# Kernel tuning notes

Hardware: AMD Instinct MI355X
Metric: run time of the kernel (lower is better)

The kernel has to match this reference:

```python
import jax, jax.numpy as jnp
import numpy as np

N_HEADS = 8
N_POINTS = 4


def _bilinear_sample(img, x, y):
    """img: (d, H, W); x, y: (P, H, W) float pixel coords (align_corners=True).
    Zero padding for out-of-bounds (matches F.grid_sample defaults).
    Returns (d, P, H, W)."""
    Hh, Ww = img.shape[1], img.shape[2]
    x0f = jnp.floor(x); y0f = jnp.floor(y)
    x0 = x0f.astype(jnp.int32); x1 = x0 + 1
    y0 = y0f.astype(jnp.int32); y1 = y0 + 1
    wx = x - x0f; wy = y - y0f

    def gather(yi, xi):
        valid = (yi >= 0) & (yi < Hh) & (xi >= 0) & (xi < Ww)
        yc = jnp.clip(yi, 0, Hh - 1)
        xc = jnp.clip(xi, 0, Ww - 1)
        v = img[:, yc, xc]  # (d, P, H, W)
        return v * valid[None].astype(img.dtype)

    out = (gather(y0, x0) * ((1 - wy) * (1 - wx))[None]
           + gather(y0, x1) * ((1 - wy) * wx)[None]
           + gather(y1, x0) * (wy * (1 - wx))[None]
           + gather(y1, x1) * (wy * wx)[None])
    return out


def _forward(query, key, W_off, b_off, W_proj, b_proj):
    B, C, H, W = query.shape
    nh, npts = N_HEADS, N_POINTS
    dh = C // nh
    N = H * W

    # offsets + weights from flattened query tokens
    qf = query.reshape(B, C, N).transpose(0, 2, 1)            # (B, N, C)
    ow = qf @ W_off + b_off                                    # (B, N, nh*npts*3)
    ow = ow.reshape(B, H, W, nh, npts, 3)
    offsets = ow[..., :2]                                      # (B,H,W,nh,npts,2)
    weights = jax.nn.softmax(ow[..., 2], axis=-1)              # (B,H,W,nh,npts)

    # base grid in [-1, 1], (x, y) order
    gy = jnp.linspace(-1.0, 1.0, H, dtype=query.dtype)
    gx = jnp.linspace(-1.0, 1.0, W, dtype=query.dtype)
    gyy, gxx = jnp.meshgrid(gy, gx, indexing='ij')             # (H, W)
    grid = jnp.stack([gxx, gyy], axis=-1)                      # (H, W, 2)

    locs = grid[None, :, :, None, None, :] + offsets * 0.1     # (B,H,W,nh,npts,2)
    locs = locs.transpose(0, 3, 4, 1, 2, 5)                    # (B,nh,npts,H,W,2)
    locs = locs.reshape(B * nh, npts, H, W, 2)

    # normalized -> pixel coords (align_corners=True)
    xpix = (locs[..., 0] + 1.0) * 0.5 * (W - 1)                # (B*nh, npts, H, W)
    ypix = (locs[..., 1] + 1.0) * 0.5 * (H - 1)

    key_r = key.reshape(B * nh, dh, H, W)
    sampled = jax.vmap(_bilinear_sample)(key_r, xpix, ypix)    # (B*nh, dh, npts, H, W)
    sampled = sampled.reshape(B, nh, dh, npts, H, W).transpose(0, 1, 3, 2, 4, 5)  # (B,nh,npts,dh,H,W)

    w = weights.transpose(0, 3, 4, 1, 2)[:, :, :, None, :, :]  # (B,nh,npts,1,H,W)
    out_feat = (sampled * w).sum(axis=2)                       # (B,nh,dh,H,W)
    out_feat = out_feat.reshape(B, C, N).transpose(0, 2, 1)    # (B,N,C)
    return out_feat @ W_proj + b_proj                          # (B,N,C)


def setup_inputs() -> dict:
    key0 = jax.random.key(0)
    ks = jax.random.split(key0, 6)
    B, C, H, W = 8, 256, 64, 64
    query = jax.random.normal(ks[0], (B, C, H, W), dtype=jnp.float32)
    key = jax.random.normal(ks[1], (B, C, H, W), dtype=jnp.float32)
    # small random offset net so sampling deviates from base grid (orig inits to 0)
    W_off = jax.random.normal(ks[2], (C, N_HEADS * N_POINTS * 3), dtype=jnp.float32) * 0.01
    b_off = jax.random.normal(ks[3], (N_HEADS * N_POINTS * 3,), dtype=jnp.float32) * 0.01
    W_proj = jax.random.normal(ks[4], (C, C), dtype=jnp.float32) * (1.0 / np.sqrt(C))
    b_proj = jnp.zeros((C,), dtype=jnp.float32)
    return {"query": query, "key": key, "W_off": W_off, "b_off": b_off,
            "W_proj": W_proj, "b_proj": b_proj}


def reference(query, key, W_off, b_off, W_proj, b_proj):
    return _forward(query, key, W_off, b_off, W_proj, b_proj)
```

## Files before the change

### kernel.cpp

```cpp
#include <hip/hip_runtime.h>

#define NH   8
#define NPTS 4
#define BB   8
#define CCH  256
#define HH   64
#define WW   64
#define NPIX 4096
#define DH   32

__global__ __launch_bounds__(256)
void kA_gemm(const float* __restrict__ query, const float* __restrict__ W_off,
             const float* __restrict__ b_off, float4* __restrict__ coords)
{
    __shared__ float a_lds[64][68];
    __shared__ float w_lds[64][100];

    const int t    = threadIdx.x;
    const int bid  = blockIdx.x;
    const int sbid = (bid & 7) * 64 + (bid >> 3);
    const int m0   = sbid * 64;
    const int b    = m0 >> 12;
    const int n0   = m0 & (NPIX - 1);
    const float* qbase = query + (size_t)b * CCH * NPIX + n0;

    const int kg = t >> 7;
    const int tl = t & 127;
    const int tm = tl >> 3;
    const int tj = tl & 7;

    float acc[4][12];
#pragma unroll
    for (int i = 0; i < 4; ++i)
#pragma unroll
        for (int j = 0; j < 12; ++j) acc[i][j] = 0.f;

    for (int kc = 0; kc < 128; kc += 32) {
        float4 a[4];
#pragma unroll
        for (int ii = 0; ii < 4; ++ii) {
            const int idx = t + ii * 256;
            const int lr = idx >> 4, m4 = idx & 15;
            const int gk = ((lr >> 5) << 7) + kc + (lr & 31);
            a[ii] = *(const float4*)(qbase + (size_t)gk * NPIX + (m4 << 2));
        }
        float4 w[6];
#pragma unroll
        for (int ii = 0; ii < 6; ++ii) {
            const int idx = t + ii * 256;
            const int lr = idx / 24, q = idx - lr * 24;
            const int gk = ((lr >> 5) << 7) + kc + (lr & 31);
            w[ii] = *(const float4*)(W_off + (size_t)gk * 96 + (q << 2));
        }
        __syncthreads();
#pragma unroll
        for (int ii = 0; ii < 4; ++ii) {
            const int idx = t + ii * 256;
            *(float4*)&a_lds[idx >> 4][(idx & 15) << 2] = a[ii];
        }
#pragma unroll
        for (int ii = 0; ii < 6; ++ii) {
            const int idx = t + ii * 256;
            const int lr = idx / 24, q = idx - lr * 24;
            *(float4*)&w_lds[lr][q << 2] = w[ii];
        }
        __syncthreads();

        const int kr0 = kg << 5;
#pragma unroll
        for (int kk = 0; kk < 32; ++kk) {
            const int kr = kr0 + kk;
            const float4 av = *(const float4*)&a_lds[kr][tm << 2];
            const float4 w0 = *(const float4*)&w_lds[kr][tj * 12];
            const float4 w1 = *(const float4*)&w_lds[kr][tj * 12 + 4];
            const float4 w2 = *(const float4*)&w_lds[kr][tj * 12 + 8];
            const float ar[4]  = {av.x, av.y, av.z, av.w};
            const float wr[12] = {w0.x, w0.y, w0.z, w0.w,
                                  w1.x, w1.y, w1.z, w1.w,
                                  w2.x, w2.y, w2.z, w2.w};
#pragma unroll
            for (int i = 0; i < 4; ++i)
#pragma unroll
                for (int j = 0; j < 12; ++j)
                    acc[i][j] = fmaf(ar[i], wr[j], acc[i][j]);
        }
    }

    __syncthreads();
    if (kg == 0) {
#pragma unroll
        for (int i = 0; i < 4; ++i)
#pragma unroll
            for (int jq = 0; jq < 3; ++jq) {
                float4 v = make_float4(acc[i][jq * 4 + 0], acc[i][jq * 4 + 1],
                                       acc[i][jq * 4 + 2], acc[i][jq * 4 + 3]);
                *(float4*)&w_lds[(tm << 2) + i][tj * 12 + (jq << 2)] = v;
            }
    }
    __syncthreads();
    if (kg == 1) {
#pragma unroll
        for (int i = 0; i < 4; ++i)
#pragma unroll
            for (int jq = 0; jq < 3; ++jq) {
                const float4 v = *(const float4*)&w_lds[(tm << 2) + i][tj * 12 + (jq << 2)];
                acc[i][jq * 4 + 0] += v.x;
                acc[i][jq * 4 + 1] += v.y;
                acc[i][jq * 4 + 2] += v.z;
                acc[i][jq * 4 + 3] += v.w;
            }

        float bo[12];
#pragma unroll
        for (int j = 0; j < 12; ++j) bo[j] = b_off[tj * 12 + j];

#pragma unroll
        for (int i = 0; i < 4; ++i) {
            const int g = m0 + (tm << 2) + i;
            const int n = g & (NPIX - 1);
            const float fx = (float)(n & 63), fy = (float)(n >> 6);

            float ox[4], oy[4], l[4];
#pragma unroll
            for (int p = 0; p < 4; ++p) {
                ox[p] = acc[i][p * 3 + 0] + bo[p * 3 + 0];
                oy[p] = acc[i][p * 3 + 1] + bo[p * 3 + 1];
                l[p]  = acc[i][p * 3 + 2] + bo[p * 3 + 2];
            }
            float m = fmaxf(fmaxf(l[0], l[1]), fmaxf(l[2], l[3]));
            float e[4], s = 0.f;
#pragma unroll
            for (int p = 0; p < 4; ++p) { e[p] = __expf(l[p] - m); s += e[p]; }
            const float inv = 1.f / s;

            float4* cp = coords + ((size_t)g * NH + tj) * NPTS;
#pragma unroll
            for (int p = 0; p < 4; ++p)
                cp[p] = make_float4(fx + ox[p] * 3.15f, fy + oy[p] * 3.15f,
                                    e[p] * inv, 0.f);
        }
    }
}

__global__ __launch_bounds__(256)
void kT_transpose(const float* __restrict__ key, float* __restrict__ keyT)
{
    __shared__ float tile[64][65];
    int bid = blockIdx.x;
    const int nt = bid & 63; bid >>= 6;
    const int ct = bid & 3;  bid >>= 2;
    const int b  = bid;
    const int n0 = nt * 64, c0 = ct * 64;
    const int t = threadIdx.x;

    const float* src = key + ((size_t)b * CCH + c0) * NPIX + n0;
#pragma unroll
    for (int ii = 0; ii < 4; ++ii) {
        int idx = t + ii * 256;
        int cc = idx >> 4, q = idx & 15;
        float4 v = *(const float4*)(src + (size_t)cc * NPIX + (q << 2));
        tile[cc][(q << 2) + 0] = v.x;
        tile[cc][(q << 2) + 1] = v.y;
        tile[cc][(q << 2) + 2] = v.z;
        tile[cc][(q << 2) + 3] = v.w;
    }
    __syncthreads();
    float* dst = keyT + ((size_t)(b * NPIX + n0)) * CCH + c0;
#pragma unroll
    for (int ii = 0; ii < 4; ++ii) {
        int idx = t + ii * 256;
        int nn = idx >> 4, q = idx & 15;
        float4 v = make_float4(tile[(q << 2) + 0][nn], tile[(q << 2) + 1][nn],
                               tile[(q << 2) + 2][nn], tile[(q << 2) + 3][nn]);
        *(float4*)(dst + (size_t)nn * CCH + (q << 2)) = v;
    }
}

__global__ __launch_bounds__(256)
void kB_gather(const float* __restrict__ keyT, const float4* __restrict__ coords,
               float* __restrict__ feat)
{
    const int bid  = blockIdx.x;
    const int sbid = (bid & 7) * 1024 + (bid >> 3);

    const int t  = threadIdx.x;
    const int wv = t >> 6, l = t & 63;
    const int g  = sbid * 4 + wv;
    const int b  = g >> 12;
    const int head = l >> 3;
    const int cl   = (l & 7) << 2;
    const int c    = head * DH + cl;

    const float*  kb = keyT + (((size_t)b << 12)) * CCH;
    const float4* cp = coords + ((size_t)g * NH + head) * NPTS;

    float4 acc = make_float4(0.f, 0.f, 0.f, 0.f);
#pragma unroll
    for (int pt = 0; pt < 4; ++pt) {
        float4 co = cp[pt];
        float xp = co.x, yp = co.y, wgt = co.z;
        float x0f = floorf(xp), y0f = floorf(yp);
        int   x0  = (int)x0f,  y0  = (int)y0f;
        float wx  = xp - x0f,  wy  = yp - y0f;
#pragma unroll
        for (int cr = 0; cr < 4; ++cr) {
            int   xi = x0 + (cr & 1);
            int   yi = y0 + (cr >> 1);
            float wc = ((cr & 1) ? wx : 1.f - wx) * ((cr >> 1) ? wy : 1.f - wy);
            bool  valid = (xi >= 0) && (xi < WW) && (yi >= 0) && (yi < HH);
            int   xc = min(max(xi, 0), WW - 1);
            int   yc = min(max(yi, 0), HH - 1);
            float ww = valid ? (wgt * wc) : 0.f;
            float4 v = *(const float4*)(kb + ((size_t)((yc << 6) + xc)) * CCH + c);
            acc.x = fmaf(ww, v.x, acc.x);
            acc.y = fmaf(ww, v.y, acc.y);
            acc.z = fmaf(ww, v.z, acc.z);
            acc.w = fmaf(ww, v.w, acc.w);
        }
    }
    *(float4*)(feat + (size_t)g * CCH + c) = acc;
}

__global__ __launch_bounds__(256)
void kB_sample(const float* __restrict__ key, const float4* __restrict__ coords,
               float* __restrict__ feat)
{
    __shared__ float cx[4][64], cy[4][64], cw[4][64];

    const int t = threadIdx.x;
    int bi = blockIdx.x;
    const int y    = bi & 63; bi >>= 6;
    const int head = bi & 7;  bi >>= 3;
    const int b    = bi;

    {
        const int xx = t >> 2, pt = t & 3;
        float4 v = coords[((size_t)(b * NPIX + y * WW + xx) * NH + head) * NPTS + pt];
        cx[pt][xx] = v.x; cy[pt][xx] = v.y; cw[pt][xx] = v.z;
    }
    __syncthreads();

    const int x  = t & 63;
    const int cg = t >> 6;
    const int c0 = head * DH + cg * 8;
    const float* kbase = key + ((size_t)b * CCH + c0) * NPIX;

    float acc[8];
#pragma unroll
    for (int i = 0; i < 8; ++i) acc[i] = 0.f;

#pragma unroll
    for (int pt = 0; pt < 4; ++pt) {
        float xp = cx[pt][x], yp = cy[pt][x], wgt = cw[pt][x];
        float x0f = floorf(xp), y0f = floorf(yp);
        int   x0  = (int)x0f,  y0  = (int)y0f;
        float wx  = xp - x0f,  wy  = yp - y0f;
#pragma unroll
        for (int cr = 0; cr < 4; ++cr) {
            int   xi = x0 + (cr & 1);
            int   yi = y0 + (cr >> 1);
            float wc = ((cr & 1) ? wx : 1.f - wx) * ((cr >> 1) ? wy : 1.f - wy);
            bool  valid = (xi >= 0) && (xi < WW) && (yi >= 0) && (yi < HH);
            int   xc = min(max(xi, 0), WW - 1);
            int   yc = min(max(yi, 0), HH - 1);
            const float* p = kbase + yc * WW + xc;
            float ww = valid ? (wgt * wc) : 0.f;
#pragma unroll
            for (int c = 0; c < 8; ++c)
                acc[c] = fmaf(ww, p[(size_t)c * NPIX], acc[c]);
        }
    }

    float* fp = feat + (size_t)(b * NPIX + y * WW + x) * CCH + c0;
    *(float4*)fp       = make_float4(acc[0], acc[1], acc[2], acc[3]);
    *(float4*)(fp + 4) = make_float4(acc[4], acc[5], acc[6], acc[7]);
}

__global__ __launch_bounds__(256)
void kC_proj(const float* __restrict__ feat, const float* __restrict__ W_proj,
             const float* __restrict__ b_proj, float* __restrict__ out)
{
    __shared__ float a_lds[64][36];
    __shared__ float b_lds[32][128];

    const int t    = threadIdx.x;
    const int bid  = blockIdx.x;
    const int sbid = (bid & 7) * 128 + (bid >> 3);
    const int mb = sbid >> 1;
    const int nb = sbid & 1;
    const int m0 = mb * 64, n0 = nb * 128;

    const int tm = t >> 4, tn = t & 15;

    float acc[4][8];
#pragma unroll
    for (int i = 0; i < 4; ++i)
#pragma unroll
        for (int j = 0; j < 8; ++j) acc[i][j] = 0.f;

    for (int kc = 0; kc < 256; kc += 32) {
        float4 a[2];
#pragma unroll
        for (int ii = 0; ii < 2; ++ii) {
            const int idx = t + ii * 256;
            a[ii] = *(const float4*)(feat + (size_t)(m0 + (idx >> 3)) * 256
                                     + kc + ((idx & 7) << 2));
        }
        float4 w[4];
#pragma unroll
        for (int ii = 0; ii < 4; ++ii) {
            const int idx = t + ii * 256;
            w[ii] = *(const float4*)(W_proj + (size_t)(kc + (idx >> 5)) * 256
                                     + n0 + ((idx & 31) << 2));
        }
        __syncthreads();
#pragma unroll
        for (int ii = 0; ii < 2; ++ii) {
            const int idx = t + ii * 256;
            *(float4*)&a_lds[idx >> 3][(idx & 7) << 2] = a[ii];
        }
#pragma unroll
        for (int ii = 0; ii < 4; ++ii) {
            const int idx = t + ii * 256;
            *(float4*)&b_lds[idx >> 5][(idx & 31) << 2] = w[ii];
        }
        __syncthreads();
#pragma unroll
        for (int k4 = 0; k4 < 8; ++k4) {
            float ar[4][4];
#pragma unroll
            for (int i = 0; i < 4; ++i) {
                const float4 av = *(const float4*)&a_lds[(tm << 2) + i][k4 << 2];
                ar[i][0] = av.x; ar[i][1] = av.y; ar[i][2] = av.z; ar[i][3] = av.w;
            }
#pragma unroll
            for (int kk = 0; kk < 4; ++kk) {
                const int k = (k4 << 2) + kk;
                const float4 bv0 = *(const float4*)&b_lds[k][tn << 2];
                const float4 bv1 = *(const float4*)&b_lds[k][64 + (tn << 2)];
                const float br[8] = {bv0.x, bv0.y, bv0.z, bv0.w,
                                     bv1.x, bv1.y, bv1.z, bv1.w};
#pragma unroll
                for (int i = 0; i < 4; ++i)
#pragma unroll
                    for (int j = 0; j < 8; ++j)
                        acc[i][j] = fmaf(ar[i][kk], br[j], acc[i][j]);
            }
        }
    }

    const float4 bp0 = *(const float4*)(b_proj + n0 + (tn << 2));
    const float4 bp1 = *(const float4*)(b_proj + n0 + 64 + (tn << 2));
#pragma unroll
    for (int i = 0; i < 4; ++i) {
        float* op = out + (size_t)(m0 + (tm << 2) + i) * 256 + n0;
        *(float4*)(op + (tn << 2)) =
            make_float4(acc[i][0] + bp0.x, acc[i][1] + bp0.y,
                        acc[i][2] + bp0.z, acc[i][3] + bp0.w);
        *(float4*)(op + 64 + (tn << 2)) =
            make_float4(acc[i][4] + bp1.x, acc[i][5] + bp1.y,
                        acc[i][6] + bp1.z, acc[i][7] + bp1.w);
    }
}

extern "C" void kernel_launch(void* const* d_in, const int* in_sizes, int n_in,
                              void* d_out, int out_size, void* d_ws, size_t ws_size,
                              hipStream_t stream)
{
    const float* query  = (const float*)d_in[0];
    const float* key    = (const float*)d_in[1];
    const float* W_off  = (const float*)d_in[2];
    const float* b_off  = (const float*)d_in[3];
    const float* W_proj = (const float*)d_in[4];
    const float* b_proj = (const float*)d_in[5];
    float* out = (float*)d_out;

    const size_t keyT_bytes   = (size_t)BB * NPIX * CCH * sizeof(float);
    const size_t coords_bytes = (size_t)BB * NPIX * NH * NPTS * sizeof(float4);
    const size_t feat_bytes   = (size_t)BB * NPIX * CCH * sizeof(float);

    if (ws_size >= keyT_bytes + coords_bytes + feat_bytes) {
        float*  keyT   = (float*)d_ws;
        float4* coords = (float4*)((char*)d_ws + keyT_bytes);
        float*  feat   = (float*)((char*)d_ws + keyT_bytes + coords_bytes);

        kA_gemm<<<(BB * NPIX) / 64, 256, 0, stream>>>(query, W_off, b_off, coords);
        kT_transpose<<<BB * 4 * 64, 256, 0, stream>>>(key, keyT);
        kB_gather<<<(BB * NPIX) / 4, 256, 0, stream>>>(keyT, coords, feat);
        kC_proj<<<(BB * NPIX / 64) * 2, 256, 0, stream>>>(feat, W_proj, b_proj, out);
    } else {
        float4* coords = (float4*)d_ws;
        float*  feat   = (float*)((char*)d_ws + coords_bytes);

        kA_gemm<<<(BB * NPIX) / 64, 256, 0, stream>>>(query, W_off, b_off, coords);
        kB_sample<<<BB * NH * HH, 256, 0, stream>>>(key, coords, feat);
        kC_proj<<<(BB * NPIX / 64) * 2, 256, 0, stream>>>(feat, W_proj, b_proj, out);
    }
}
```

Before: 269.9 us.

## Use split-bf16 MFMA for output projection and drop fallback sampler path

Replaces the FP32 SIMT output-projection GEMM with a bf16 MFMA kernel that keeps roughly FP32 accuracy by splitting each operand into high and low bf16 parts and summing three products. The gather kernel now writes the features as bf16 high/low halves, and a small new kernel transposes and splits W_proj, reusing the keyT workspace once the gather has finished. This aims to move the projection's arithmetic onto the matrix cores and cut bytes read from feat, at the cost of three MFMAs per tile and an extra launch. The smaller-workspace fallback path is removed, so the code now assumes the workspace is large enough.

```diff
diff --git a/kernel.cpp b/kernel.cpp
--- a/kernel.cpp
+++ b/kernel.cpp
@@ -1,4 +1,5 @@
 #include <hip/hip_runtime.h>
+#include <hip/hip_bf16.h>
 
 #define NH   8
 #define NPTS 4
@@ -8,6 +9,16 @@
 #define WW   64
 #define NPIX 4096
 #define DH   32
+
+typedef __attribute__((ext_vector_type(8))) short bf16x8;
+typedef __attribute__((ext_vector_type(4))) float f32x4;
+
+__device__ __forceinline__ ushort f2bf(float x) {
+    union { __hip_bfloat16 b; ushort u; } c; c.b = __float2bfloat16(x); return c.u;
+}
+__device__ __forceinline__ float bf2f(ushort u) {
+    union { __hip_bfloat16 b; ushort u; } c; c.u = u; return __bfloat162float(c.b);
+}
 
 __global__ __launch_bounds__(256)
 void kA_gemm(const float* __restrict__ query, const float* __restrict__ W_off,
@@ -120,17 +131,17 @@
             const int n = g & (NPIX - 1);
             const float fx = (float)(n & 63), fy = (float)(n >> 6);
 
-            float ox[4], oy[4], l[4];
+            float ox[4], oy[4], lg[4];
 #pragma unroll
             for (int p = 0; p < 4; ++p) {
                 ox[p] = acc[i][p * 3 + 0] + bo[p * 3 + 0];
                 oy[p] = acc[i][p * 3 + 1] + bo[p * 3 + 1];
-                l[p]  = acc[i][p * 3 + 2] + bo[p * 3 + 2];
+                lg[p] = acc[i][p * 3 + 2] + bo[p * 3 + 2];
             }
-            float m = fmaxf(fmaxf(l[0], l[1]), fmaxf(l[2], l[3]));
+            float m = fmaxf(fmaxf(lg[0], lg[1]), fmaxf(lg[2], lg[3]));
             float e[4], s = 0.f;
 #pragma unroll
-            for (int p = 0; p < 4; ++p) { e[p] = __expf(l[p] - m); s += e[p]; }
+            for (int p = 0; p < 4; ++p) { e[p] = __expf(lg[p] - m); s += e[p]; }
             const float inv = 1.f / s;
 
             float4* cp = coords + ((size_t)g * NH + tj) * NPTS;
@@ -178,7 +189,7 @@
 
 __global__ __launch_bounds__(256)
 void kB_gather(const float* __restrict__ keyT, const float4* __restrict__ coords,
-               float* __restrict__ feat)
+               ushort* __restrict__ featH, ushort* __restrict__ featL)
 {
     const int bid  = blockIdx.x;
     const int sbid = (bid & 7) * 1024 + (bid >> 3);
@@ -218,148 +229,141 @@
             acc.w = fmaf(ww, v.w, acc.w);
         }
     }
-    *(float4*)(feat + (size_t)g * CCH + c) = acc;
+    const float a4[4] = {acc.x, acc.y, acc.z, acc.w};
+    ushort hs[4], ls[4];
+#pragma unroll
+    for (int j = 0; j < 4; ++j) {
+        hs[j] = f2bf(a4[j]);
+        ls[j] = f2bf(a4[j] - bf2f(hs[j]));
+    }
+    *(ushort4*)(featH + (size_t)g * CCH + c) = make_ushort4(hs[0], hs[1], hs[2], hs[3]);
+    *(ushort4*)(featL + (size_t)g * CCH + c) = make_ushort4(ls[0], ls[1], ls[2], ls[3]);
 }
 
 __global__ __launch_bounds__(256)
-void kB_sample(const float* __restrict__ key, const float4* __restrict__ coords,
-               float* __restrict__ feat)
-{
-    __shared__ float cx[4][64], cy[4][64], cw[4][64];
-
-    const int t = threadIdx.x;
-    int bi = blockIdx.x;
-    const int y    = bi & 63; bi >>= 6;
-    const int head = bi & 7;  bi >>= 3;
-    const int b    = bi;
-
-    {
-        const int xx = t >> 2, pt = t & 3;
-        float4 v = coords[((size_t)(b * NPIX + y * WW + xx) * NH + head) * NPTS + pt];
-        cx[pt][xx] = v.x; cy[pt][xx] = v.y; cw[pt][xx] = v.z;
+void kW_conv(const float* __restrict__ W, ushort* __restrict__ WTh,
+             ushort* __restrict__ WTl)
+{
+    __shared__ float tile[64][65];
+    const int t  = threadIdx.x;
+    const int kt = blockIdx.x >> 2, nt = blockIdx.x & 3;
+    const int k0 = kt * 64, n0 = nt * 64;
+
+    const float* src = W + (size_t)k0 * 256 + n0;
+#pragma unroll
+    for (int ii = 0; ii < 4; ++ii) {
+        int idx = t + ii * 256;
+        int kk = idx >> 4, q = idx & 15;
+        float4 v = *(const float4*)(src + (size_t)kk * 256 + (q << 2));
+        tile[kk][(q << 2) + 0] = v.x;
+        tile[kk][(q << 2) + 1] = v.y;
+        tile[kk][(q << 2) + 2] = v.z;
+        tile[kk][(q << 2) + 3] = v.w;
     }
     __syncthreads();
-
-    const int x  = t & 63;
-    const int cg = t >> 6;
-    const int c0 = head * DH + cg * 8;
-    const float* kbase = key + ((size_t)b * CCH + c0) * NPIX;
-
-    float acc[8];
-#pragma unroll
-    for (int i = 0; i < 8; ++i) acc[i] = 0.f;
-
-#pragma unroll
-    for (int pt = 0; pt < 4; ++pt) {
-        float xp = cx[pt][x], yp = cy[pt][x], wgt = cw[pt][x];
-        float x0f = floorf(xp), y0f = floorf(yp);
-        int   x0  = (int)x0f,  y0  = (int)y0f;
-        float wx  = xp - x0f,  wy  = yp - y0f;
-#pragma unroll
-        for (int cr = 0; cr < 4; ++cr) {
-            int   xi = x0 + (cr & 1);
-            int   yi = y0 + (cr >> 1);
-            float wc = ((cr & 1) ? wx : 1.f - wx) * ((cr >> 1) ? wy : 1.f - wy);
-            bool  valid = (xi >= 0) && (xi < WW) && (yi >= 0) && (yi < HH);
-            int   xc = min(max(xi, 0), WW - 1);
-            int   yc = min(max(yi, 0), HH - 1);
-            const float* p = kbase + yc * WW + xc;
-            float ww = valid ? (wgt * wc) : 0.f;
-#pragma unroll
-            for (int c = 0; c < 8; ++c)
-                acc[c] = fmaf(ww, p[(size_t)c * NPIX], acc[c]);
-        }
-    }
-
-    float* fp = feat + (size_t)(b * NPIX + y * WW + x) * CCH + c0;
-    *(float4*)fp       = make_float4(acc[0], acc[1], acc[2], acc[3]);
-    *(float4*)(fp + 4) = make_float4(acc[4], acc[5], acc[6], acc[7]);
+#pragma unroll
+    for (int ii = 0; ii < 4; ++ii) {
+        int idx = t + ii * 256;
+        int nn = idx >> 4, q = idx & 15;
+        float xs[4] = { tile[(q << 2) + 0][nn], tile[(q << 2) + 1][nn],
+                        tile[(q << 2) + 2][nn], tile[(q << 2) + 3][nn] };
+        ushort hs[4], ls[4];
+#pragma unroll
+        for (int j = 0; j < 4; ++j) {
+            hs[j] = f2bf(xs[j]);
+            ls[j] = f2bf(xs[j] - bf2f(hs[j]));
+        }
+        *(ushort4*)(WTh + (size_t)(n0 + nn) * 256 + k0 + (q << 2)) =
+            make_ushort4(hs[0], hs[1], hs[2], hs[3]);
+        *(ushort4*)(WTl + (size_t)(n0 + nn) * 256 + k0 + (q << 2)) =
+            make_ushort4(ls[0], ls[1], ls[2], ls[3]);
+    }
 }
 
 __global__ __launch_bounds__(256)
-void kC_proj(const float* __restrict__ feat, const float* __restrict__ W_proj,
+void kC_mfma(const ushort* __restrict__ featH, const ushort* __restrict__ featL,
+             const ushort* __restrict__ WTh, const ushort* __restrict__ WTl,
              const float* __restrict__ b_proj, float* __restrict__ out)
 {
-    __shared__ float a_lds[64][36];
-    __shared__ float b_lds[32][128];
-
-    const int t    = threadIdx.x;
-    const int bid  = blockIdx.x;
-    const int sbid = (bid & 7) * 128 + (bid >> 3);
-    const int mb = sbid >> 1;
-    const int nb = sbid & 1;
-    const int m0 = mb * 64, n0 = nb * 128;
-
-    const int tm = t >> 4, tn = t & 15;
-
-    float acc[4][8];
+    __shared__ __align__(16) ushort Ah[128][40];
+    __shared__ __align__(16) ushort Al[128][40];
+    __shared__ __align__(16) ushort Bh[128][40];
+    __shared__ __align__(16) ushort Bl[128][40];
+
+    const int t  = threadIdx.x;
+    const int mb = blockIdx.x >> 1;
+    const int nb = blockIdx.x & 1;
+    const int m0 = mb * 128, n0 = nb * 128;
+    const int w  = t >> 6, l = t & 63;
+    const int wr = w >> 1, wc = w & 1;
+    const int lr = l & 15;
+    const int lk = (l >> 4) << 3;
+
+    f32x4 acc[4][4];
 #pragma unroll
     for (int i = 0; i < 4; ++i)
 #pragma unroll
-        for (int j = 0; j < 8; ++j) acc[i][j] = 0.f;
+        for (int j = 0; j < 4; ++j) acc[i][j] = (f32x4){0.f, 0.f, 0.f, 0.f};
 
     for (int kc = 0; kc < 256; kc += 32) {
-        float4 a[2];
+        uint4 ra[2], rla[2], rb[2], rlb[2];
 #pragma unroll
         for (int ii = 0; ii < 2; ++ii) {
             const int idx = t + ii * 256;
-            a[ii] = *(const float4*)(feat + (size_t)(m0 + (idx >> 3)) * 256
-                                     + kc + ((idx & 7) << 2));
-        }
-        float4 w[4];
-#pragma unroll
-        for (int ii = 0; ii < 4; ++ii) {
-            const int idx = t + ii * 256;
-            w[ii] = *(const float4*)(W_proj + (size_t)(kc + (idx >> 5)) * 256
-                                     + n0 + ((idx & 31) << 2));
+            const int row = idx >> 2, q = idx & 3;
+            ra[ii]  = *(const uint4*)(featH + (size_t)(m0 + row) * 256 + kc + (q << 3));
+            rla[ii] = *(const uint4*)(featL + (size_t)(m0 + row) * 256 + kc + (q << 3));
+            rb[ii]  = *(const uint4*)(WTh   + (size_t)(n0 + row) * 256 + kc + (q << 3));
+            rlb[ii] = *(const uint4*)(WTl   + (size_t)(n0 + row) * 256 + kc + (q << 3));
         }
         __syncthreads();
 #pragma unroll
         for (int ii = 0; ii < 2; ++ii) {
             const int idx = t + ii * 256;
-            *(float4*)&a_lds[idx >> 3][(idx & 7) << 2] = a[ii];
-        }
-#pragma unroll
-        for (int ii = 0; ii < 4; ++ii) {
-            const int idx = t + ii * 256;
-            *(float4*)&b_lds[idx >> 5][(idx & 31) << 2] = w[ii];
+            const int row = idx >> 2, q = idx & 3;
+            *(uint4*)&Ah[row][q << 3] = ra[ii];
+            *(uint4*)&Al[row][q << 3] = rla[ii];
+            *(uint4*)&Bh[row][q << 3] = rb[ii];
+            *(uint4*)&Bl[row][q << 3] = rlb[ii];
         }
         __syncthreads();
-#pragma unroll
-        for (int k4 = 0; k4 < 8; ++k4) {
-            float ar[4][4];
-#pragma unroll
-            for (int i = 0; i < 4; ++i) {
-                const float4 av = *(const float4*)&a_lds[(tm << 2) + i][k4 << 2];
-                ar[i][0] = av.x; ar[i][1] = av.y; ar[i][2] = av.z; ar[i][3] = av.w;
+
+        bf16x8 fb[4], fbl[4];
+#pragma unroll
+        for (int nf = 0; nf < 4; ++nf) {
+            fb[nf]  = *(const bf16x8*)&Bh[wc * 64 + nf * 16 + lr][lk];
+            fbl[nf] = *(const bf16x8*)&Bl[wc * 64 + nf * 16 + lr][lk];
+        }
+#pragma unroll
+        for (int mf = 0; mf < 4; ++mf) {
+            const bf16x8 fa  = *(const bf16x8*)&Ah[wr * 64 + mf * 16 + lr][lk];
+            const bf16x8 fal = *(const bf16x8*)&Al[wr * 64 + mf * 16 + lr][lk];
+#pragma unroll
+            for (int nf = 0; nf < 4; ++nf) {
+                acc[mf][nf] = __builtin_amdgcn_mfma_f32_16x16x32_bf16(
+                                  fa, fb[nf], acc[mf][nf], 0, 0, 0);
+                acc[mf][nf] = __builtin_amdgcn_mfma_f32_16x16x32_bf16(
+                                  fa, fbl[nf], acc[mf][nf], 0, 0, 0);
+                acc[mf][nf] = __builtin_amdgcn_mfma_f32_16x16x32_bf16(
+                                  fal, fb[nf], acc[mf][nf], 0, 0, 0);
             }
-#pragma unroll
-            for (int kk = 0; kk < 4; ++kk) {
-                const int k = (k4 << 2) + kk;
-                const float4 bv0 = *(const float4*)&b_lds[k][tn << 2];
-                const float4 bv1 = *(const float4*)&b_lds[k][64 + (tn << 2)];
-                const float br[8] = {bv0.x, bv0.y, bv0.z, bv0.w,
-                                     bv1.x, bv1.y, bv1.z, bv1.w};
-#pragma unroll
-                for (int i = 0; i < 4; ++i)
-#pragma unroll
-                    for (int j = 0; j < 8; ++j)
-                        acc[i][j] = fmaf(ar[i][kk], br[j], acc[i][j]);
-            }
-        }
-    }
-
-    const float4 bp0 = *(const float4*)(b_proj + n0 + (tn << 2));
-    const float4 bp1 = *(const float4*)(b_proj + n0 + 64 + (tn << 2));
-#pragma unroll
-    for (int i = 0; i < 4; ++i) {
-        float* op = out + (size_t)(m0 + (tm << 2) + i) * 256 + n0;
-        *(float4*)(op + (tn << 2)) =
-            make_float4(acc[i][0] + bp0.x, acc[i][1] + bp0.y,
-                        acc[i][2] + bp0.z, acc[i][3] + bp0.w);
-        *(float4*)(op + 64 + (tn << 2)) =
-            make_float4(acc[i][4] + bp1.x, acc[i][5] + bp1.y,
-                        acc[i][6] + bp1.z, acc[i][7] + bp1.w);
+        }
+    }
+
+    const int r4 = (l >> 4) << 2;
+#pragma unroll
+    for (int nf = 0; nf < 4; ++nf) {
+        const int col = n0 + wc * 64 + nf * 16 + lr;
+        const float bp = b_proj[col];
+#pragma unroll
+        for (int mf = 0; mf < 4; ++mf) {
+            const int row = m0 + wr * 64 + mf * 16 + r4;
+            const f32x4 v = acc[mf][nf];
+            out[(size_t)(row + 0) * 256 + col] = v.x + bp;
+            out[(size_t)(row + 1) * 256 + col] = v.y + bp;
+            out[(size_t)(row + 2) * 256 + col] = v.z + bp;
+            out[(size_t)(row + 3) * 256 + col] = v.w + bp;
+        }
     }
 }
 
@@ -377,23 +381,20 @@
 
     const size_t keyT_bytes   = (size_t)BB * NPIX * CCH * sizeof(float);
     const size_t coords_bytes = (size_t)BB * NPIX * NH * NPTS * sizeof(float4);
-    const size_t feat_bytes   = (size_t)BB * NPIX * CCH * sizeof(float);
-
-    if (ws_size >= keyT_bytes + coords_bytes + feat_bytes) {
-        float*  keyT   = (float*)d_ws;
-        float4* coords = (float4*)((char*)d_ws + keyT_bytes);
-        float*  feat   = (float*)((char*)d_ws + keyT_bytes + coords_bytes);
-
-        kA_gemm<<<(BB * NPIX) / 64, 256, 0, stream>>>(query, W_off, b_off, coords);
-        kT_transpose<<<BB * 4 * 64, 256, 0, stream>>>(key, keyT);
-        kB_gather<<<(BB * NPIX) / 4, 256, 0, stream>>>(keyT, coords, feat);
-        kC_proj<<<(BB * NPIX / 64) * 2, 256, 0, stream>>>(feat, W_proj, b_proj, out);
-    } else {
-        float4* coords = (float4*)d_ws;
-        float*  feat   = (float*)((char*)d_ws + coords_bytes);
-
-        kA_gemm<<<(BB * NPIX) / 64, 256, 0, stream>>>(query, W_off, b_off, coords);
-        kB_sample<<<BB * NH * HH, 256, 0, stream>>>(key, coords, feat);
-        kC_proj<<<(BB * NPIX / 64) * 2, 256, 0, stream>>>(feat, W_proj, b_proj, out);
-    }
-}
+    const size_t feat_bytes   = (size_t)BB * NPIX * CCH * sizeof(ushort);
+
+    char* p = (char*)d_ws;
+    float*  keyT   = (float*)p;
+    ushort* WTh    = (ushort*)p;
+    ushort* WTl    = (ushort*)(p + 131072);
+    float4* coords = (float4*)(p + keyT_bytes);
+    ushort* featH  = (ushort*)(p + keyT_bytes + coords_bytes);
+    ushort* featL  = (ushort*)(p + keyT_bytes + coords_bytes + feat_bytes);
+
+    kA_gemm<<<(BB * NPIX) / 64, 256, 0, stream>>>(query, W_off, b_off, coords);
+    kT_transpose<<<BB * 4 * 64, 256, 0, stream>>>(key, keyT);
+    kB_gather<<<(BB * NPIX) / 4, 256, 0, stream>>>(keyT, coords, featH, featL);
+    kW_conv<<<16, 256, 0, stream>>>(W_proj, WTh, WTl);
+    kC_mfma<<<(BB * NPIX / 128) * 2, 256, 0, stream>>>(featH, featL, WTh, WTl,
+                                                       b_proj, out);
+}
```

New measurement: 236.2 us. 12.5% less time.
